# Kernel tuning notes

Hardware: AMD Instinct MI355X
Metric: run time of the kernel (lower is better)

## Reference

```python
import jax, jax.numpy as jnp
import numpy as np

N = 50000      # nodes
E = 1600000    # edges (before self loops)
IN = 128       # in_channels
HID = 64       # hidden_channels
OUT = 16       # out_channels
NEG_SLOPE = 0.2


def gat_conv(x, edge_index, W, a_src, a_dst, bias, heads, ch):
    """PyG GATConv: linear -> per-edge attention (LeakyReLU) -> segment softmax
    over destination nodes -> scatter-add aggregation. add_self_loops=True."""
    n = x.shape[0]
    loop = jnp.arange(n, dtype=edge_index.dtype)
    src = jnp.concatenate([edge_index[0], loop])  # [Etot]
    dst = jnp.concatenate([edge_index[1], loop])
    h = (x @ W).reshape(n, heads, ch)             # [N,H,C]
    asrc = jnp.sum(h * a_src, axis=-1)            # [N,H]
    adst = jnp.sum(h * a_dst, axis=-1)            # [N,H]
    e = jax.nn.leaky_relu(asrc[src] + adst[dst], NEG_SLOPE)      # [Etot,H]
    emax = jax.ops.segment_max(e, dst, num_segments=n)           # [N,H]
    emax = jnp.where(jnp.isfinite(emax), emax, 0.0)
    p = jnp.exp(e - emax[dst])
    denom = jax.ops.segment_sum(p, dst, num_segments=n)          # [N,H]
    alpha = p / (denom[dst] + 1e-16)                             # [Etot,H]
    out = jax.ops.segment_sum(h[src] * alpha[:, :, None], dst, num_segments=n)
    return out.reshape(n, heads * ch) + bias      # concat (heads=1 is a no-op)


def setup_inputs() -> dict:
    key = jax.random.key(0)
    ks = jax.random.split(key, 12)
    s = 0.05
    return {
        "x": jax.random.normal(ks[0], (N, IN), dtype=jnp.float32),
        "edge_index": jax.random.randint(ks[1], (2, E), 0, N, dtype=jnp.int64),
        # conv1: heads=2
        "W1": jax.random.normal(ks[2], (IN, 2 * HID), dtype=jnp.float32) * s,
        "a_src1": jax.random.normal(ks[3], (2, HID), dtype=jnp.float32) * s,
        "a_dst1": jax.random.normal(ks[4], (2, HID), dtype=jnp.float32) * s,
        "b1": jnp.zeros((2 * HID,), dtype=jnp.float32),
        # conv2: heads=1, in = 2*HID
        "W2": jax.random.normal(ks[5], (2 * HID, HID), dtype=jnp.float32) * s,
        "a_src2": jax.random.normal(ks[6], (1, HID), dtype=jnp.float32) * s,
        "a_dst2": jax.random.normal(ks[7], (1, HID), dtype=jnp.float32) * s,
        "b2": jnp.zeros((HID,), dtype=jnp.float32),
        # final linear
        "Wl": jax.random.normal(ks[8], (HID, OUT), dtype=jnp.float32) * s,
        "bl": jnp.zeros((OUT,), dtype=jnp.float32),
    }


def reference(x, edge_index, W1, a_src1, a_dst1, b1, W2, a_src2, a_dst2, b2, Wl, bl):
    h = jax.nn.relu(gat_conv(x, edge_index, W1, a_src1, a_dst1, b1, heads=2, ch=HID))
    # dropout p=0.3: identity at inference (deterministic reference)
    h = jax.nn.relu(gat_conv(h, edge_index, W2, a_src2, a_dst2, b2, heads=1, ch=HID))
    return h @ Wl + bl
```

## Files before the change

kernel.cpp:

```cpp
#include <hip/hip_runtime.h>
#include <hip/hip_fp16.h>

#define NEG 0.2f
#define RW 512
#define RSH 9
#define RCAP 18432


template <int K, int M, int H, bool PART>
__global__ __launch_bounds__(256) void k_gemm(const float* __restrict__ X,
                                              const float* __restrict__ W,
                                              const float* __restrict__ a_src,
                                              const float* __restrict__ a_dst,
                                              __half* __restrict__ Yh,
                                              float* __restrict__ asrc,
                                              float* __restrict__ adst, int n,
                                              const int* __restrict__ esrc,
                                              const int* __restrict__ edst, int E, int NRg,
                                              int* rcur, unsigned int* part) {
    constexpr int KH = 32;
    constexpr int NQ = M / 64;
    __shared__ float Ws[KH * M];
    __shared__ float Xs[64][K + 4];
    int tid = threadIdx.x;
    int row0 = blockIdx.x * 64;

    if (PART && blockIdx.x * 2048 < E) {
        __shared__ int ph[128];
        __shared__ int pb[128];
        int i0 = (blockIdx.x * 256 + tid) * 8;
        int ds[8], ss[8];
        if (i0 + 7 < E) {
            int4 a = *reinterpret_cast<const int4*>(&edst[i0]);
            int4 b = *reinterpret_cast<const int4*>(&edst[i0 + 4]);
            ds[0] = a.x; ds[1] = a.y; ds[2] = a.z; ds[3] = a.w;
            ds[4] = b.x; ds[5] = b.y; ds[6] = b.z; ds[7] = b.w;
            int4 c = *reinterpret_cast<const int4*>(&esrc[i0]);
            int4 d = *reinterpret_cast<const int4*>(&esrc[i0 + 4]);
            ss[0] = c.x; ss[1] = c.y; ss[2] = c.z; ss[3] = c.w;
            ss[4] = d.x; ss[5] = d.y; ss[6] = d.z; ss[7] = d.w;
        } else {
#pragma unroll
            for (int j = 0; j < 8; j++) {
                ds[j] = (i0 + j < E) ? edst[i0 + j] : 0;
                ss[j] = (i0 + j < E) ? esrc[i0 + j] : 0;
            }
        }
        if (tid < NRg) ph[tid] = 0;
        __syncthreads();
#pragma unroll
        for (int j = 0; j < 8; j++)
            if (i0 + j < E) atomicAdd(&ph[ds[j] >> RSH], 1);
        __syncthreads();
        if (tid < NRg) {
            int c = ph[tid];
            pb[tid] = c ? atomicAdd(&rcur[tid], c) : 0;
            ph[tid] = 0;
        }
        __syncthreads();
#pragma unroll
        for (int j = 0; j < 8; j++) {
            if (i0 + j < E) {
                int r = ds[j] >> RSH;
                int rk = atomicAdd(&ph[r], 1) + pb[r];
                if (rk < RCAP)
                    part[(size_t)r * RCAP + rk] =
                        ((unsigned int)(ds[j] & (RW - 1)) << 16) | (unsigned int)(ss[j] & 0xFFFF);
            }
        }
    }

    for (int idx = tid; idx < 64 * (K / 4); idx += 256) {
        int r = idx / (K / 4), c4 = idx % (K / 4);
        int gr = row0 + r;
        float4 v = make_float4(0.f, 0.f, 0.f, 0.f);
        if (gr < n) v = *reinterpret_cast<const float4*>(&X[(size_t)gr * K + c4 * 4]);
        *reinterpret_cast<float4*>(&Xs[r][c4 * 4]) = v;
    }

    int rg = tid >> 4;
    int cq = tid & 15;

    float4 acc[4][NQ];
#pragma unroll
    for (int j = 0; j < 4; j++)
#pragma unroll
        for (int qi = 0; qi < NQ; qi++) acc[j][qi] = make_float4(0.f, 0.f, 0.f, 0.f);

    for (int kh = 0; kh < K; kh += KH) {
        __syncthreads();
        for (int idx = tid; idx < (KH * M) / 4; idx += 256) {
            *reinterpret_cast<float4*>(&Ws[idx * 4]) =
                *reinterpret_cast<const float4*>(&W[(size_t)kh * M + idx * 4]);
        }
        __syncthreads();
#pragma unroll 1
        for (int k4 = 0; k4 < KH; k4 += 4) {
            float4 x0 = *reinterpret_cast<const float4*>(&Xs[rg * 4 + 0][kh + k4]);
            float4 x1 = *reinterpret_cast<const float4*>(&Xs[rg * 4 + 1][kh + k4]);
            float4 x2 = *reinterpret_cast<const float4*>(&Xs[rg * 4 + 2][kh + k4]);
            float4 x3 = *reinterpret_cast<const float4*>(&Xs[rg * 4 + 3][kh + k4]);
#pragma unroll
            for (int kk = 0; kk < 4; kk++) {
                float xs0 = kk == 0 ? x0.x : kk == 1 ? x0.y : kk == 2 ? x0.z : x0.w;
                float xs1 = kk == 0 ? x1.x : kk == 1 ? x1.y : kk == 2 ? x1.z : x1.w;
                float xs2 = kk == 0 ? x2.x : kk == 1 ? x2.y : kk == 2 ? x2.z : x2.w;
                float xs3 = kk == 0 ? x3.x : kk == 1 ? x3.y : kk == 2 ? x3.z : x3.w;
#pragma unroll
                for (int qi = 0; qi < NQ; qi++) {
                    float4 wv =
                        *reinterpret_cast<const float4*>(&Ws[(k4 + kk) * M + (cq + 16 * qi) * 4]);
                    acc[0][qi].x += xs0 * wv.x; acc[0][qi].y += xs0 * wv.y;
                    acc[0][qi].z += xs0 * wv.z; acc[0][qi].w += xs0 * wv.w;
                    acc[1][qi].x += xs1 * wv.x; acc[1][qi].y += xs1 * wv.y;
                    acc[1][qi].z += xs1 * wv.z; acc[1][qi].w += xs1 * wv.w;
                    acc[2][qi].x += xs2 * wv.x; acc[2][qi].y += xs2 * wv.y;
                    acc[2][qi].z += xs2 * wv.z; acc[2][qi].w += xs2 * wv.w;
                    acc[3][qi].x += xs3 * wv.x; acc[3][qi].y += xs3 * wv.y;
                    acc[3][qi].z += xs3 * wv.z; acc[3][qi].w += xs3 * wv.w;
                }
            }
        }
    }

#pragma unroll
    for (int j = 0; j < 4; j++) {
        int gr = row0 + rg * 4 + j;
        if (gr < n) {
#pragma unroll
            for (int qi = 0; qi < NQ; qi++) {
                union {
                    __half2 h2[2];
                    uint2 u;
                } cv;
                cv.h2[0] = __floats2half2_rn(acc[j][qi].x, acc[j][qi].y);
                cv.h2[1] = __floats2half2_rn(acc[j][qi].z, acc[j][qi].w);
                *reinterpret_cast<uint2*>(&Yh[(size_t)gr * M + (cq + 16 * qi) * 4]) = cv.u;
            }
        }
    }

    float4 av0 = *reinterpret_cast<const float4*>(&a_src[cq * 4]);
    float4 dv0 = *reinterpret_cast<const float4*>(&a_dst[cq * 4]);
    float4 av1 = av0, dv1 = dv0;
    if (NQ == 2) {
        av1 = *reinterpret_cast<const float4*>(&a_src[(cq + 16) * 4]);
        dv1 = *reinterpret_cast<const float4*>(&a_dst[(cq + 16) * 4]);
    }
#pragma unroll
    for (int j = 0; j < 4; j++) {
        float s0 = acc[j][0].x * av0.x + acc[j][0].y * av0.y + acc[j][0].z * av0.z +
                   acc[j][0].w * av0.w;
        float d0 = acc[j][0].x * dv0.x + acc[j][0].y * dv0.y + acc[j][0].z * dv0.z +
                   acc[j][0].w * dv0.w;
        float s1 = 0.f, d1 = 0.f;
        if (NQ == 2) {
            s1 = acc[j][1].x * av1.x + acc[j][1].y * av1.y + acc[j][1].z * av1.z +
                 acc[j][1].w * av1.w;
            d1 = acc[j][1].x * dv1.x + acc[j][1].y * dv1.y + acc[j][1].z * dv1.z +
                 acc[j][1].w * dv1.w;
        }
#pragma unroll
        for (int m = 1; m < 16; m <<= 1) {
            s0 += __shfl_xor(s0, m, 64);
            d0 += __shfl_xor(d0, m, 64);
            if (NQ == 2) {
                s1 += __shfl_xor(s1, m, 64);
                d1 += __shfl_xor(d1, m, 64);
            }
        }
        int gr = row0 + rg * 4 + j;
        if (cq == 0 && gr < n) {
            if (H == 2) {
                *reinterpret_cast<float2*>(&asrc[gr * 2]) = make_float2(s0, s1);
                *reinterpret_cast<float2*>(&adst[gr * 2]) = make_float2(d0, d1);
            } else {
                asrc[gr] = s0;
                adst[gr] = d0;
            }
        }
    }
}


__global__ __launch_bounds__(512) void k_build(const unsigned int* __restrict__ part,
                                               const int* __restrict__ rcur, int n,
                                               unsigned short* __restrict__ csr,
                                               int* __restrict__ rowptr) {
    __shared__ int hist[RW];
    __shared__ int wsum[8];
    __shared__ int rbase_s;
    int r = blockIdx.x;
    int tid = threadIdx.x, lane = tid & 63, wid = tid >> 6;
    int cnt = min(rcur[r], RCAP);
    if (tid == 0) {
        int b = 0;
        for (int j = 0; j < r; j++) b += min(rcur[j], RCAP);
        rbase_s = b;
    }
    hist[tid] = 0;
    __syncthreads();
    int rbase = rbase_s;
    const unsigned int* pr = part + (size_t)r * RCAP;

    for (int i = tid; i < cnt; i += 512) atomicAdd(&hist[pr[i] >> 16], 1);
    __syncthreads();

    int v = hist[tid];
    int incl = v;
#pragma unroll
    for (int m = 1; m < 64; m <<= 1) {
        int t = __shfl_up(incl, m, 64);
        if (lane >= m) incl += t;
    }
    if (lane == 63) wsum[wid] = incl;
    __syncthreads();
    if (wid == 0) {
        int s = (lane < 8) ? wsum[lane] : 0;
#pragma unroll
        for (int m = 1; m < 8; m <<= 1) {
            int t = __shfl_up(s, m, 64);
            if (lane >= m) s += t;
        }
        if (lane < 8) wsum[lane] = s;
    }
    __syncthreads();
    int excl = (incl - v) + (wid > 0 ? wsum[wid - 1] : 0);
    __syncthreads();
    hist[tid] = excl;
    int g = r * RW + tid;
    if (g < n) rowptr[g] = rbase + excl;
    if (r == gridDim.x - 1 && tid == 0) rowptr[n] = rbase + cnt;
    __syncthreads();

    for (int i = tid; i < cnt; i += 512) {
        unsigned int e = pr[i];
        int rk = atomicAdd(&hist[e >> 16], 1);
        csr[rbase + rk] = (unsigned short)(e & 0xFFFF);
    }
}


__global__ __launch_bounds__(256) void k_gat2(const __half* __restrict__ hh,
                                              const float* __restrict__ asrc,
                                              const float* __restrict__ adst,
                                              const int* __restrict__ rowptr,
                                              const unsigned short* __restrict__ csr_src,
                                              const float* __restrict__ bias,
                                              float* __restrict__ out, int n) {
    int node = blockIdx.x * 4 + (threadIdx.x >> 6);
    int lane = threadIdx.x & 63;
    if (node >= n) return;

    int beg = rowptr[node], end = rowptr[node + 1];
    float2 adn = *reinterpret_cast<const float2*>(&adst[node * 2]);
    float2 asn = *reinterpret_cast<const float2*>(&asrc[node * 2]);
    float e0 = asn.x + adn.x;
    e0 = e0 > 0.f ? e0 : NEG * e0;
    float e1 = asn.y + adn.y;
    e1 = e1 > 0.f ? e1 : NEG * e1;
    float pself0 = __expf(e0), pself1 = __expf(e1);

    int g = lane >> 4;
    int lc = lane & 15;
    bool head1 = lc >= 8;

    float4 sraw = *reinterpret_cast<const float4*>(&hh[(size_t)node * 128 + lc * 8]);

    float2 acc[4];
#pragma unroll
    for (int k = 0; k < 4; k++) acc[k] = make_float2(0.f, 0.f);
    float psum0 = 0.f, psum1 = 0.f;

    for (int base = beg; base < end; base += 64) {
        int i = base + lane;
        int cnt = min(64, end - base);
        float p0 = 0.f, p1 = 0.f;
        int s = 0;
        if (i < end) {
            s = (int)csr_src[i];
            float2 a2 = *reinterpret_cast<const float2*>(&asrc[s * 2]);
            float f0 = a2.x + adn.x;
            f0 = f0 > 0.f ? f0 : NEG * f0;
            float f1 = a2.y + adn.y;
            f1 = f1 > 0.f ? f1 : NEG * f1;
            p0 = __expf(f0);
            p1 = __expf(f1);
            psum0 += p0;
            psum1 += p1;
        }
        int nt = (cnt + 3) >> 2;
#pragma unroll 8
        for (int t = 0; t < nt; t++) {
            int ej = t * 4 + g;
            int sj = __shfl(s, ej, 64);
            float pj0 = __shfl(p0, ej, 64);
            float pj1 = __shfl(p1, ej, 64);
            float pj = head1 ? pj1 : pj0;
            if (ej < cnt) {
                float4 raw = *reinterpret_cast<const float4*>(&hh[(size_t)sj * 128 + lc * 8]);
                const __half2* hp = reinterpret_cast<const __half2*>(&raw);
#pragma unroll
                for (int k = 0; k < 4; k++) {
                    float2 f = __half22float2(hp[k]);
                    acc[k].x += pj * f.x;
                    acc[k].y += pj * f.y;
                }
            }
        }
    }

#pragma unroll
    for (int m = 1; m < 64; m <<= 1) {
        psum0 += __shfl_xor(psum0, m, 64);
        psum1 += __shfl_xor(psum1, m, 64);
    }
    float inv0 = 1.f / (psum0 + pself0 + 1e-16f);
    float inv1 = 1.f / (psum1 + pself1 + 1e-16f);

#pragma unroll
    for (int m = 16; m < 64; m <<= 1) {
#pragma unroll
        for (int k = 0; k < 4; k++) {
            acc[k].x += __shfl_xor(acc[k].x, m, 64);
            acc[k].y += __shfl_xor(acc[k].y, m, 64);
        }
    }

    float inv = head1 ? inv1 : inv0;
    float pself = head1 ? pself1 : pself0;
    const __half2* sp = reinterpret_cast<const __half2*>(&sraw);
    float4 b0 = *reinterpret_cast<const float4*>(&bias[lc * 8]);
    float4 b1 = *reinterpret_cast<const float4*>(&bias[lc * 8 + 4]);
    float o[8];
#pragma unroll
    for (int k = 0; k < 4; k++) {
        float2 f = __half22float2(sp[k]);
        o[2 * k] = (acc[k].x + pself * f.x) * inv;
        o[2 * k + 1] = (acc[k].y + pself * f.y) * inv;
    }
    o[0] = fmaxf(o[0] + b0.x, 0.f);
    o[1] = fmaxf(o[1] + b0.y, 0.f);
    o[2] = fmaxf(o[2] + b0.z, 0.f);
    o[3] = fmaxf(o[3] + b0.w, 0.f);
    o[4] = fmaxf(o[4] + b1.x, 0.f);
    o[5] = fmaxf(o[5] + b1.y, 0.f);
    o[6] = fmaxf(o[6] + b1.z, 0.f);
    o[7] = fmaxf(o[7] + b1.w, 0.f);

    if (lane < 16) {
        float* op = &out[(size_t)node * 128 + lc * 8];
        *reinterpret_cast<float4*>(op) = make_float4(o[0], o[1], o[2], o[3]);
        *reinterpret_cast<float4*>(op + 4) = make_float4(o[4], o[5], o[6], o[7]);
    }
}


__global__ __launch_bounds__(256) void k_gat1(const __half* __restrict__ hh,
                                              const float* __restrict__ asrc,
                                              const float* __restrict__ adst,
                                              const int* __restrict__ rowptr,
                                              const unsigned short* __restrict__ csr_src,
                                              const float* __restrict__ bias,
                                              const float* __restrict__ Wl,
                                              const float* __restrict__ bl,
                                              float* __restrict__ out, int n) {
    __shared__ float Wls[64 * 16];
    __shared__ float bls[16];
    __shared__ float hbuf[4][64];
    int tid = threadIdx.x;
    for (int i = tid; i < 64 * 16; i += 256) Wls[i] = Wl[i];
    if (tid < 16) bls[tid] = bl[tid];
    __syncthreads();

    int w = tid >> 6, lane = tid & 63;
    int node = blockIdx.x * 4 + w;
    if (node >= n) return;

    int beg = rowptr[node], end = rowptr[node + 1];
    float adn = adst[node];
    float e0 = asrc[node] + adn;
    e0 = e0 > 0.f ? e0 : NEG * e0;
    float pself = __expf(e0);

    int g = lane >> 3;
    int lc = lane & 7;

    float4 sraw = *reinterpret_cast<const float4*>(&hh[(size_t)node * 64 + lc * 8]);

    float2 acc[4];
#pragma unroll
    for (int k = 0; k < 4; k++) acc[k] = make_float2(0.f, 0.f);
    float psum = 0.f;

    for (int base = beg; base < end; base += 64) {
        int i = base + lane;
        int cnt = min(64, end - base);
        float p = 0.f;
        int s = 0;
        if (i < end) {
            s = (int)csr_src[i];
            float e = asrc[s] + adn;
            e = e > 0.f ? e : NEG * e;
            p = __expf(e);
            psum += p;
        }
        int nt = (cnt + 7) >> 3;
#pragma unroll 8
        for (int t = 0; t < nt; t++) {
            int ej = t * 8 + g;
            int sj = __shfl(s, ej, 64);
            float pj = __shfl(p, ej, 64);
            if (ej < cnt) {
                float4 raw = *reinterpret_cast<const float4*>(&hh[(size_t)sj * 64 + lc * 8]);
                const __half2* hp = reinterpret_cast<const __half2*>(&raw);
#pragma unroll
                for (int k = 0; k < 4; k++) {
                    float2 f = __half22float2(hp[k]);
                    acc[k].x += pj * f.x;
                    acc[k].y += pj * f.y;
                }
            }
        }
    }

#pragma unroll
    for (int m = 1; m < 64; m <<= 1) psum += __shfl_xor(psum, m, 64);
    float inv = 1.f / (psum + pself + 1e-16f);

#pragma unroll
    for (int m = 8; m < 64; m <<= 1) {
#pragma unroll
        for (int k = 0; k < 4; k++) {
            acc[k].x += __shfl_xor(acc[k].x, m, 64);
            acc[k].y += __shfl_xor(acc[k].y, m, 64);
        }
    }

    const __half2* sp = reinterpret_cast<const __half2*>(&sraw);
    float4 b0 = *reinterpret_cast<const float4*>(&bias[lc * 8]);
    float4 b1 = *reinterpret_cast<const float4*>(&bias[lc * 8 + 4]);
    float o[8];
#pragma unroll
    for (int k = 0; k < 4; k++) {
        float2 f = __half22float2(sp[k]);
        o[2 * k] = (acc[k].x + pself * f.x) * inv;
        o[2 * k + 1] = (acc[k].y + pself * f.y) * inv;
    }
    o[0] = fmaxf(o[0] + b0.x, 0.f);
    o[1] = fmaxf(o[1] + b0.y, 0.f);
    o[2] = fmaxf(o[2] + b0.z, 0.f);
    o[3] = fmaxf(o[3] + b0.w, 0.f);
    o[4] = fmaxf(o[4] + b1.x, 0.f);
    o[5] = fmaxf(o[5] + b1.y, 0.f);
    o[6] = fmaxf(o[6] + b1.z, 0.f);
    o[7] = fmaxf(o[7] + b1.w, 0.f);

    if (lane < 8) {
        float* hp = &hbuf[w][lc * 8];
        *reinterpret_cast<float4*>(hp) = make_float4(o[0], o[1], o[2], o[3]);
        *reinterpret_cast<float4*>(hp + 4) = make_float4(o[4], o[5], o[6], o[7]);
    }
    __builtin_amdgcn_wave_barrier();

    int col = lane & 15, q = lane >> 4;
    float a = 0.f;
#pragma unroll
    for (int k = 0; k < 16; k++) {
        int kk = q * 16 + k;
        a += hbuf[w][kk] * Wls[kk * 16 + col];
    }
    a += __shfl_xor(a, 16, 64);
    a += __shfl_xor(a, 32, 64);
    if (lane < 16) out[(size_t)node * 16 + col] = a + bls[col];
}


extern "C" void kernel_launch(void* const* d_in, const int* in_sizes, int n_in,
                              void* d_out, int out_size, void* d_ws, size_t ws_size,
                              hipStream_t stream) {
    const float* x      = (const float*)d_in[0];
    const int*   ei     = (const int*)d_in[1];
    const float* W1     = (const float*)d_in[2];
    const float* a_src1 = (const float*)d_in[3];
    const float* a_dst1 = (const float*)d_in[4];
    const float* b1     = (const float*)d_in[5];
    const float* W2     = (const float*)d_in[6];
    const float* a_src2 = (const float*)d_in[7];
    const float* a_dst2 = (const float*)d_in[8];
    const float* b2     = (const float*)d_in[9];
    const float* Wl     = (const float*)d_in[10];
    const float* bl     = (const float*)d_in[11];
    float* out = (float*)d_out;

    int n = in_sizes[0] / 128;
    int E = in_sizes[1] / 2;
    const int* src = ei;
    const int* dst = ei + E;
    int NRg = (n + RW - 1) >> RSH;

    char* w = (char*)d_ws;
    size_t off = 0;
    auto alloc = [&](size_t bytes) {
        void* p = w + off;
        off = (off + bytes + 255) & ~(size_t)255;
        return p;
    };
    int*            rcur   = (int*)alloc(128 * 4);
    unsigned int*   part   = (unsigned int*)alloc((size_t)NRg * RCAP * 4);
    int*            rowptr = (int*)alloc((size_t)(n + 1) * 4);
    unsigned short* csr    = (unsigned short*)alloc((size_t)E * 2);
    __half*         h1h    = (__half*)alloc((size_t)n * 128 * 2);
    float*          as1    = (float*)alloc((size_t)n * 2 * 4);
    float*          ad1    = (float*)alloc((size_t)n * 2 * 4);
    float*          hm     = (float*)alloc((size_t)n * 128 * 4);
    __half*         h2h    = (__half*)alloc((size_t)n * 64 * 2);
    float*          as2    = (float*)alloc((size_t)n * 4);
    float*          ad2    = (float*)alloc((size_t)n * 4);

    hipMemsetAsync(rcur, 0, 128 * 4, stream);

    int gblocks = (n + 63) / 64;
    int bblocks = (E + 2047) / 2048;
    int grid1 = gblocks > bblocks ? gblocks : bblocks;

    k_gemm<128, 128, 2, true><<<grid1, 256, 0, stream>>>(x, W1, a_src1, a_dst1, h1h, as1, ad1, n,
                                                         src, dst, E, NRg, rcur, part);
    k_build<<<NRg, 512, 0, stream>>>(part, rcur, n, csr, rowptr);
    k_gat2<<<(n + 3) / 4, 256, 0, stream>>>(h1h, as1, ad1, rowptr, csr, b1, hm, n);

    k_gemm<128, 64, 1, false><<<gblocks, 256, 0, stream>>>(hm, W2, a_src2, a_dst2, h2h, as2, ad2, n,
                                                           nullptr, nullptr, 0, 0, nullptr, nullptr);
    k_gat1<<<(n + 3) / 4, 256, 0, stream>>>(h2h, as2, ad2, rowptr, csr, b2, Wl, bl, out, n);
}
```

Measured before the change: 217.9 us.

## Split layer-1 aggregation per head and store intermediate activations in fp16

The layer-1 aggregation kernel now assigns one wavefront per (node, head) pair instead of one per node. Each lane group handles 8 edges at a time over 64 channels, which doubles the wave count and halves the per-wave gather work. The intermediate activation tensor is written as fp16 instead of fp32, and the second GEMM gains a template path that loads half inputs and converts them to float in shared memory. This halves the intermediate write and read traffic, at the cost of fp16 rounding on post-ReLU activations and duplicate CSR and attention-score reads per head.

```diff
diff --git a/kernel.cpp b/kernel.cpp
--- a/kernel.cpp
+++ b/kernel.cpp
@@ -7,8 +7,8 @@
 #define RCAP 18432
 
 
-template <int K, int M, int H, bool PART>
-__global__ __launch_bounds__(256) void k_gemm(const float* __restrict__ X,
+template <int K, int M, int H, bool PART, bool XHALF>
+__global__ __launch_bounds__(256) void k_gemm(const void* __restrict__ Xv,
                                               const float* __restrict__ W,
                                               const float* __restrict__ a_src,
                                               const float* __restrict__ a_dst,
@@ -70,12 +70,34 @@
         }
     }
 
-    for (int idx = tid; idx < 64 * (K / 4); idx += 256) {
-        int r = idx / (K / 4), c4 = idx % (K / 4);
-        int gr = row0 + r;
-        float4 v = make_float4(0.f, 0.f, 0.f, 0.f);
-        if (gr < n) v = *reinterpret_cast<const float4*>(&X[(size_t)gr * K + c4 * 4]);
-        *reinterpret_cast<float4*>(&Xs[r][c4 * 4]) = v;
+    if (XHALF) {
+        const __half* Xh = (const __half*)Xv;
+        for (int idx = tid; idx < 64 * (K / 8); idx += 256) {
+            int r = idx / (K / 8), c8 = idx % (K / 8);
+            int gr = row0 + r;
+            float4 a = make_float4(0.f, 0.f, 0.f, 0.f), b = a;
+            if (gr < n) {
+                uint4 v = *reinterpret_cast<const uint4*>(&Xh[(size_t)gr * K + c8 * 8]);
+                const __half2* hp = reinterpret_cast<const __half2*>(&v);
+                float2 f0 = __half22float2(hp[0]);
+                float2 f1 = __half22float2(hp[1]);
+                float2 f2 = __half22float2(hp[2]);
+                float2 f3 = __half22float2(hp[3]);
+                a = make_float4(f0.x, f0.y, f1.x, f1.y);
+                b = make_float4(f2.x, f2.y, f3.x, f3.y);
+            }
+            *reinterpret_cast<float4*>(&Xs[r][c8 * 8]) = a;
+            *reinterpret_cast<float4*>(&Xs[r][c8 * 8 + 4]) = b;
+        }
+    } else {
+        const float* X = (const float*)Xv;
+        for (int idx = tid; idx < 64 * (K / 4); idx += 256) {
+            int r = idx / (K / 4), c4 = idx % (K / 4);
+            int gr = row0 + r;
+            float4 v = make_float4(0.f, 0.f, 0.f, 0.f);
+            if (gr < n) v = *reinterpret_cast<const float4*>(&X[(size_t)gr * K + c4 * 4]);
+            *reinterpret_cast<float4*>(&Xs[r][c4 * 4]) = v;
+        }
     }
 
     int rg = tid >> 4;
@@ -247,58 +269,49 @@
                                               const int* __restrict__ rowptr,
                                               const unsigned short* __restrict__ csr_src,
                                               const float* __restrict__ bias,
-                                              float* __restrict__ out, int n) {
-    int node = blockIdx.x * 4 + (threadIdx.x >> 6);
+                                              __half* __restrict__ outh, int n) {
+    int wid = blockIdx.x * 4 + (threadIdx.x >> 6);
     int lane = threadIdx.x & 63;
+    int node = wid >> 1, head = wid & 1;
     if (node >= n) return;
 
     int beg = rowptr[node], end = rowptr[node + 1];
-    float2 adn = *reinterpret_cast<const float2*>(&adst[node * 2]);
-    float2 asn = *reinterpret_cast<const float2*>(&asrc[node * 2]);
-    float e0 = asn.x + adn.x;
+    float adn = adst[node * 2 + head];
+    float e0 = asrc[node * 2 + head] + adn;
     e0 = e0 > 0.f ? e0 : NEG * e0;
-    float e1 = asn.y + adn.y;
-    e1 = e1 > 0.f ? e1 : NEG * e1;
-    float pself0 = __expf(e0), pself1 = __expf(e1);
-
-    int g = lane >> 4;
-    int lc = lane & 15;
-    bool head1 = lc >= 8;
-
-    float4 sraw = *reinterpret_cast<const float4*>(&hh[(size_t)node * 128 + lc * 8]);
+    float pself = __expf(e0);
+
+    int g = lane >> 3;
+    int lc = lane & 7;
+
+    float4 sraw = *reinterpret_cast<const float4*>(&hh[(size_t)node * 128 + head * 64 + lc * 8]);
 
     float2 acc[4];
 #pragma unroll
     for (int k = 0; k < 4; k++) acc[k] = make_float2(0.f, 0.f);
-    float psum0 = 0.f, psum1 = 0.f;
+    float psum = 0.f;
 
     for (int base = beg; base < end; base += 64) {
         int i = base + lane;
         int cnt = min(64, end - base);
-        float p0 = 0.f, p1 = 0.f;
+        float p = 0.f;
         int s = 0;
         if (i < end) {
             s = (int)csr_src[i];
-            float2 a2 = *reinterpret_cast<const float2*>(&asrc[s * 2]);
-            float f0 = a2.x + adn.x;
-            f0 = f0 > 0.f ? f0 : NEG * f0;
-            float f1 = a2.y + adn.y;
-            f1 = f1 > 0.f ? f1 : NEG * f1;
-            p0 = __expf(f0);
-            p1 = __expf(f1);
-            psum0 += p0;
-            psum1 += p1;
-        }
-        int nt = (cnt + 3) >> 2;
+            float e = asrc[s * 2 + head] + adn;
+            e = e > 0.f ? e : NEG * e;
+            p = __expf(e);
+            psum += p;
+        }
+        int nt = (cnt + 7) >> 3;
 #pragma unroll 8
         for (int t = 0; t < nt; t++) {
-            int ej = t * 4 + g;
+            int ej = t * 8 + g;
             int sj = __shfl(s, ej, 64);
-            float pj0 = __shfl(p0, ej, 64);
-            float pj1 = __shfl(p1, ej, 64);
-            float pj = head1 ? pj1 : pj0;
+            float pj = __shfl(p, ej, 64);
             if (ej < cnt) {
-                float4 raw = *reinterpret_cast<const float4*>(&hh[(size_t)sj * 128 + lc * 8]);
+                float4 raw =
+                    *reinterpret_cast<const float4*>(&hh[(size_t)sj * 128 + head * 64 + lc * 8]);
                 const __half2* hp = reinterpret_cast<const __half2*>(&raw);
 #pragma unroll
                 for (int k = 0; k < 4; k++) {
@@ -311,15 +324,11 @@
     }
 
 #pragma unroll
-    for (int m = 1; m < 64; m <<= 1) {
-        psum0 += __shfl_xor(psum0, m, 64);
-        psum1 += __shfl_xor(psum1, m, 64);
-    }
-    float inv0 = 1.f / (psum0 + pself0 + 1e-16f);
-    float inv1 = 1.f / (psum1 + pself1 + 1e-16f);
-
-#pragma unroll
-    for (int m = 16; m < 64; m <<= 1) {
+    for (int m = 1; m < 64; m <<= 1) psum += __shfl_xor(psum, m, 64);
+    float inv = 1.f / (psum + pself + 1e-16f);
+
+#pragma unroll
+    for (int m = 8; m < 64; m <<= 1) {
 #pragma unroll
         for (int k = 0; k < 4; k++) {
             acc[k].x += __shfl_xor(acc[k].x, m, 64);
@@ -327,11 +336,9 @@
         }
     }
 
-    float inv = head1 ? inv1 : inv0;
-    float pself = head1 ? pself1 : pself0;
     const __half2* sp = reinterpret_cast<const __half2*>(&sraw);
-    float4 b0 = *reinterpret_cast<const float4*>(&bias[lc * 8]);
-    float4 b1 = *reinterpret_cast<const float4*>(&bias[lc * 8 + 4]);
+    float4 b0 = *reinterpret_cast<const float4*>(&bias[head * 64 + lc * 8]);
+    float4 b1 = *reinterpret_cast<const float4*>(&bias[head * 64 + lc * 8 + 4]);
     float o[8];
 #pragma unroll
     for (int k = 0; k < 4; k++) {
@@ -348,10 +355,16 @@
     o[6] = fmaxf(o[6] + b1.z, 0.f);
     o[7] = fmaxf(o[7] + b1.w, 0.f);
 
-    if (lane < 16) {
-        float* op = &out[(size_t)node * 128 + lc * 8];
-        *reinterpret_cast<float4*>(op) = make_float4(o[0], o[1], o[2], o[3]);
-        *reinterpret_cast<float4*>(op + 4) = make_float4(o[4], o[5], o[6], o[7]);
+    if (lane < 8) {
+        union {
+            __half2 h2[4];
+            uint4 u;
+        } cv;
+        cv.h2[0] = __floats2half2_rn(o[0], o[1]);
+        cv.h2[1] = __floats2half2_rn(o[2], o[3]);
+        cv.h2[2] = __floats2half2_rn(o[4], o[5]);
+        cv.h2[3] = __floats2half2_rn(o[6], o[7]);
+        *reinterpret_cast<uint4*>(&outh[(size_t)node * 128 + head * 64 + lc * 8]) = cv.u;
     }
 }
 
@@ -513,7 +526,7 @@
     __half*         h1h    = (__half*)alloc((size_t)n * 128 * 2);
     float*          as1    = (float*)alloc((size_t)n * 2 * 4);
     float*          ad1    = (float*)alloc((size_t)n * 2 * 4);
-    float*          hm     = (float*)alloc((size_t)n * 128 * 4);
+    __half*         hmh    = (__half*)alloc((size_t)n * 128 * 2);
     __half*         h2h    = (__half*)alloc((size_t)n * 64 * 2);
     float*          as2    = (float*)alloc((size_t)n * 4);
     float*          ad2    = (float*)alloc((size_t)n * 4);
@@ -524,12 +537,12 @@
     int bblocks = (E + 2047) / 2048;
     int grid1 = gblocks > bblocks ? gblocks : bblocks;
 
-    k_gemm<128, 128, 2, true><<<grid1, 256, 0, stream>>>(x, W1, a_src1, a_dst1, h1h, as1, ad1, n,
-                                                         src, dst, E, NRg, rcur, part);
+    k_gemm<128, 128, 2, true, false><<<grid1, 256, 0, stream>>>(
+        x, W1, a_src1, a_dst1, h1h, as1, ad1, n, src, dst, E, NRg, rcur, part);
     k_build<<<NRg, 512, 0, stream>>>(part, rcur, n, csr, rowptr);
-    k_gat2<<<(n + 3) / 4, 256, 0, stream>>>(h1h, as1, ad1, rowptr, csr, b1, hm, n);
-
-    k_gemm<128, 64, 1, false><<<gblocks, 256, 0, stream>>>(hm, W2, a_src2, a_dst2, h2h, as2, ad2, n,
-                                                           nullptr, nullptr, 0, 0, nullptr, nullptr);
+    k_gat2<<<(2 * n + 3) / 4, 256, 0, stream>>>(h1h, as1, ad1, rowptr, csr, b1, hmh, n);
+
+    k_gemm<128, 64, 1, false, true><<<gblocks, 256, 0, stream>>>(
+        hmh, W2, a_src2, a_dst2, h2h, as2, ad2, n, nullptr, nullptr, 0, 0, nullptr, nullptr);
     k_gat1<<<(n + 3) / 4, 256, 0, stream>>>(h2h, as2, ad2, rowptr, csr, b2, Wl, bl, out, n);
 }
```

Measured after the change: 222.3 us. 2.0% more time.
